# Optimization experiments

Measured on AMD Instinct MI355X. Metric: run time of the kernel, lower is better.

Reference implementation:

```python
import jax, jax.numpy as jnp
import numpy as np

B, T, F = 2, 128, 88          # batch, time frames, pitch bins (hard-coded 88)
HIDDEN = 64                    # LSTM input dim
N_UNIT = 64                    # channel dim (= 2 * lstm hidden 32)
N_HEAD = 4
HEAD_DIM = N_UNIT // N_HEAD    # 16
WINDOW = 7
N_LAYERS = 2
DIFF_STEPS = 100
LSTM_H = N_UNIT // 2           # 32 per direction


def setup_inputs() -> dict:
    key = jax.random.key(0)
    ks = jax.random.split(key, 12)
    s = 0.05
    inp = {
        'x': jax.random.normal(ks[0], (B, T * F, HIDDEN), jnp.float32),
        't': jax.random.randint(ks[1], (B,), 0, DIFF_STEPS, jnp.int32),
        # LSTM params, stacked [layer, direction, ...]; layer-1 input dim == 2*LSTM_H == HIDDEN
        'lstm_w_ih': s * jax.random.normal(ks[2], (N_LAYERS, 2, 4 * LSTM_H, HIDDEN), jnp.float32),
        'lstm_w_hh': s * jax.random.normal(ks[3], (N_LAYERS, 2, 4 * LSTM_H, LSTM_H), jnp.float32),
        'lstm_b_ih': s * jax.random.normal(ks[4], (N_LAYERS, 2, 4 * LSTM_H), jnp.float32),
        'lstm_b_hh': s * jax.random.normal(ks[5], (N_LAYERS, 2, 4 * LSTM_H), jnp.float32),
        # per-NA-layer params
        't_emb': s * jax.random.normal(ks[6], (N_LAYERS, DIFF_STEPS, N_UNIT), jnp.float32),
        'w_qkv': s * jax.random.normal(ks[7], (N_LAYERS, N_UNIT, 3 * N_UNIT), jnp.float32),
        'b_qkv': jnp.zeros((N_LAYERS, 3 * N_UNIT), jnp.float32),
        'rpb': s * jax.random.normal(ks[8], (N_LAYERS, N_HEAD, 2 * WINDOW - 1, 2 * WINDOW - 1), jnp.float32),
        'w_proj': s * jax.random.normal(ks[9], (N_LAYERS, N_UNIT, N_UNIT), jnp.float32),
        'b_proj': jnp.zeros((N_LAYERS, N_UNIT), jnp.float32),
    }
    return inp


def _lstm_dir(x, w_ih, w_hh, b_ih, b_hh, reverse):
    # x: [N, T, D]; pytorch gate order i, f, g, o
    N = x.shape[0]
    H = w_hh.shape[1]
    xs = jnp.swapaxes(x, 0, 1)
    if reverse:
        xs = xs[::-1]
    b = b_ih + b_hh
    def step(carry, xt):
        h, c = carry
        g = xt @ w_ih.T + h @ w_hh.T + b
        i, f, gg, o = jnp.split(g, 4, axis=-1)
        c = jax.nn.sigmoid(f) * c + jax.nn.sigmoid(i) * jnp.tanh(gg)
        h = jax.nn.sigmoid(o) * jnp.tanh(c)
        return (h, c), h
    h0 = jnp.zeros((N, H), x.dtype)
    _, hs = jax.lax.scan(step, (h0, h0), xs)
    if reverse:
        hs = hs[::-1]
    return jnp.swapaxes(hs, 0, 1)


def _bilstm(x, w_ih, w_hh, b_ih, b_hh):
    for l in range(w_ih.shape[0]):
        fwd = _lstm_dir(x, w_ih[l, 0], w_hh[l, 0], b_ih[l, 0], b_hh[l, 0], False)
        bwd = _lstm_dir(x, w_ih[l, 1], w_hh[l, 1], b_ih[l, 1], b_hh[l, 1], True)
        x = jnp.concatenate([fwd, bwd], axis=-1)
    return x


def _nbh(L, w):
    # NATTEN-style clamped (non-shrinking) neighborhood window per axis
    i = jnp.arange(L)
    start = jnp.clip(i - w // 2, 0, L - w)
    idx = start[:, None] + jnp.arange(w)[None, :]   # [L, w] absolute neighbor idx
    rel = idx - i[:, None] + (w - 1)                # [L, w] rel-pos-bias idx in [0, 2w-2]
    return idx, rel


def _na2d(x, t_idx, emb, wqkv, bqkv, rpb_l, wproj, bproj):
    # x: [B, Th, Tw, C]; diffusion-step conditioning via learned embedding add
    Bx, Th, Tw, C = x.shape
    h = x + emb[t_idx][:, None, None, :]
    qkv = (h @ wqkv + bqkv).reshape(Bx, Th, Tw, 3, N_HEAD, HEAD_DIM)
    q = jnp.moveaxis(qkv[..., 0, :, :], 3, 1) * (HEAD_DIM ** -0.5)  # [B,h,Th,Tw,d]
    k = jnp.moveaxis(qkv[..., 1, :, :], 3, 1)
    v = jnp.moveaxis(qkv[..., 2, :, :], 3, 1)
    ih, rh = _nbh(Th, WINDOW)
    iw, rw = _nbh(Tw, WINDOW)
    # gather windowed neighbors: [B,h,Th,Tw,w,w,d]
    kn = k[:, :, ih[:, None, :, None], iw[None, :, None, :], :]
    vn = v[:, :, ih[:, None, :, None], iw[None, :, None, :], :]
    bias = rpb_l[:, rh[:, None, :, None], rw[None, :, None, :]]     # [h,Th,Tw,w,w]
    logits = jnp.einsum('bhijd,bhijkld->bhijkl', q, kn) + bias[None]
    attn = jax.nn.softmax(logits.reshape(Bx, N_HEAD, Th, Tw, -1), axis=-1).reshape(logits.shape)
    out = jnp.einsum('bhijkl,bhijkld->bhijd', attn, vn)             # [B,h,Th,Tw,d]
    out = jnp.moveaxis(out, 1, 3).reshape(Bx, Th, Tw, C)
    return out @ wproj + bproj


def reference(x, t, lstm_w_ih, lstm_w_hh, lstm_b_ih, lstm_b_hh,
              t_emb, w_qkv, b_qkv, rpb, w_proj, b_proj):
    Bx = x.shape[0]
    Hin = x.shape[-1]
    Tt = x.shape[1] // F
    h = x.reshape(Bx, Tt, F, Hin).transpose(0, 2, 1, 3).reshape(Bx * F, Tt, Hin)
    h = _bilstm(h, lstm_w_ih, lstm_w_hh, lstm_b_ih, lstm_b_hh)      # [B*88, T, n_unit]
    # -> [B, T, 88, n_unit] 2D grid (height=T, width=88)
    h = h.reshape(Bx, F, Tt, N_UNIT).transpose(0, 2, 1, 3)
    for l in range(N_LAYERS):
        h = h + _na2d(h, t, t_emb[l], w_qkv[l], b_qkv[l], rpb[l], w_proj[l], b_proj[l])
    return h
```

## Files before the change

### kernel.cpp

```cpp
#include <hip/hip_runtime.h>
#include <math.h>

#define B_ 2
#define T_ 128
#define F_ 88
#define HID 64
#define NU 64
#define NH 4
#define HD 16
#define LH 32
#define NSEQ (B_*F_)
#define NTOK (B_*T_*F_)
#define NPOS (T_*F_)

__device__ __forceinline__ float fsig(float x) {
    return __builtin_amdgcn_rcpf(1.0f + __expf(-x));
}
__device__ __forceinline__ float ftanh(float x) {
    return 2.0f * __builtin_amdgcn_rcpf(1.0f + __expf(-2.0f*x)) - 1.0f;
}
__device__ __forceinline__ float rdlane(float v, int l) {
    return __uint_as_float(__builtin_amdgcn_readlane(__float_as_uint(v), l));
}

template<int LAYER>
__global__ void __launch_bounds__(256, 2) gg_kernel(
    const float* __restrict__ xin,
    const float* __restrict__ w_ih,
    const float* __restrict__ b_ih,
    const float* __restrict__ b_hh,
    float* __restrict__ G)
{
    __shared__ __align__(16) float xts[32][68];
    __shared__ __align__(16) float wsh[256][68];
    __shared__ float bsh[256];
    const int s  = blockIdx.x;
    const int t0 = blockIdx.y * 32;
    const int b = s / F_, f = s % F_;
    const int tid = threadIdx.x;

    for (int n = tid; n < 32*64; n += 256) {
        const int tt = n >> 6, k = n & 63;
        xts[tt][k] = (LAYER == 0)
            ? xin[(((size_t)b*T_ + t0+tt)*F_ + f)*HID + k]
            : xin[((size_t)s*T_ + t0+tt)*HID + k];
    }
    for (int n = tid; n < 256*64; n += 256) {
        const int row = n >> 6, k = n & 63;
        wsh[row][k] = w_ih[((size_t)LAYER*256 + row)*HID + k];
    }
    bsh[tid] = b_ih[LAYER*256 + tid] + b_hh[LAYER*256 + tid];
    __syncthreads();

    const int lane = tid & 63;
    const int g    = tid >> 6;
    const int dir  = g >> 1;
    const int th   = g & 1;
    const int rowA = dir*128 + lane;
    const int rowB = dir*128 + 64 + lane;

    float accA[16] = {}, accB[16] = {};
    #pragma unroll 4
    for (int k4 = 0; k4 < 16; k4++) {
        const float4 wA = *(const float4*)&wsh[rowA][k4*4];
        const float4 wB = *(const float4*)&wsh[rowB][k4*4];
        #pragma unroll
        for (int tt = 0; tt < 16; tt++) {
            const float4 xv = *(const float4*)&xts[th*16+tt][k4*4];
            accA[tt] += wA.x*xv.x + wA.y*xv.y + wA.z*xv.z + wA.w*xv.w;
            accB[tt] += wB.x*xv.x + wB.y*xv.y + wB.z*xv.z + wB.w*xv.w;
        }
    }
    const float bA = bsh[rowA], bB = bsh[rowB];
    float2* gout = (float2*)G + ((size_t)(s*2+dir)*T_ + t0 + th*16)*64 + lane;
    #pragma unroll
    for (int tt = 0; tt < 16; tt++) {
        float2 o; o.x = accA[tt] + bA; o.y = accB[tt] + bB;
        gout[(size_t)tt*64] = o;
    }
}

template<int LAYER>
__global__ void __launch_bounds__(128, 1) lstm_rec(
    const float* __restrict__ G,
    const float* __restrict__ w_hh,
    float* __restrict__ outp)
{
    __shared__ float hbuf[T_][NU];
    const int s = blockIdx.x;
    const int b = s / F_, f = s % F_;
    const int lane = threadIdx.x & 63;
    const int dir  = threadIdx.x >> 6;

    float2 wh2[LH];
    {
        const float4* pa = (const float4*)(w_hh + ((size_t)(LAYER*2+dir)*128 + lane)*LH);
        const float4* pb = (const float4*)(w_hh + ((size_t)(LAYER*2+dir)*128 + 64 + lane)*LH);
        #pragma unroll
        for (int k4 = 0; k4 < LH/4; k4++) {
            float4 a = pa[k4], c4 = pb[k4];
            wh2[k4*4+0].x=a.x; wh2[k4*4+0].y=c4.x;
            wh2[k4*4+1].x=a.y; wh2[k4*4+1].y=c4.y;
            wh2[k4*4+2].x=a.z; wh2[k4*4+2].y=c4.z;
            wh2[k4*4+3].x=a.w; wh2[k4*4+3].y=c4.w;
        }
    }
    const float2* gp = (const float2*)G + (size_t)(s*2+dir)*T_*64 + lane;
    #define GTIME(st) (dir ? (T_-1-(st)) : (st))

    const float a1 = (lane < LH) ? 2.f : 1.f;
    const float c1 = (lane < LH) ? -1.f : 0.f;

    float h = 0.f, c = 0.f;

    #define STEP(gAv, gBv, stepi)                                            \
    {                                                                        \
        float aA0 = (gAv), aB0 = (gBv), aA1 = 0.f, aB1 = 0.f;                \
        _Pragma("unroll")                                                    \
        for (int k = 0; k < 16; k++) {                                       \
            const float hk  = rdlane(h, k);                                  \
            const float hk2 = rdlane(h, k+16);                               \
            aA0 += wh2[k].x*hk;      aB0 += wh2[k].y*hk;                     \
            aA1 += wh2[k+16].x*hk2;  aB1 += wh2[k+16].y*hk2;                 \
        }                                                                    \
        const float accA = aA0 + aA1, accB = aB0 + aB1;                      \
        const float e0 = fsig(accA);                      \
        const float e1 = fmaf(a1, fsig(a1*accB), c1);     \
        const float x0 = __shfl_xor(e0, 32, 64);        \
        const float x1 = __shfl_xor(e1, 32, 64);        \
        c = x0*c + e0*e1;                                                    \
        h = x1 * ftanh(c);                                                   \
        if (lane < LH) hbuf[GTIME(stepi)][dir*LH + lane] = h;                \
    }

    float2 A[4], Bf[4];
    #pragma unroll
    for (int i = 0; i < 4; i++) A[i]  = gp[(size_t)GTIME(i)*64];
    #pragma unroll
    for (int i = 0; i < 4; i++) Bf[i] = gp[(size_t)GTIME(4+i)*64];

    #pragma unroll 1
    for (int grp = 0; grp < 32; grp++) {
        float2 P[4];
        const int pf = (grp < 30 ? grp + 2 : 31) * 4;
        #pragma unroll
        for (int i = 0; i < 4; i++) P[i] = gp[(size_t)GTIME(pf+i)*64];
        #pragma unroll
        for (int i = 0; i < 4; i++) { STEP(A[i].x, A[i].y, grp*4 + i); }
        #pragma unroll
        for (int i = 0; i < 4; i++) { A[i] = Bf[i]; Bf[i] = P[i]; }
    }
    #undef STEP
    #undef GTIME
    __syncthreads();

    const int tid = threadIdx.x;
    const float4* lds4 = (const float4*)&hbuf[0][0];
    if (LAYER == 0) {
        float4* out4 = (float4*)outp + (size_t)s*T_*16;
        #pragma unroll
        for (int it = 0; it < 16; it++)
            out4[it*128 + tid] = lds4[it*128 + tid];
    } else {
        const int c4 = tid & 15, trow = tid >> 4;
        #pragma unroll
        for (int it = 0; it < 16; it++) {
            const int t = it*8 + trow;
            ((float4*)outp)[(((size_t)b*T_ + t)*F_ + f)*16 + c4] = lds4[t*16 + c4];
        }
    }
}

__global__ void __launch_bounds__(256, 2) qkv_kernel(
    const float* __restrict__ hcur,
    const int*   __restrict__ tarr,
    const float* __restrict__ t_emb,
    const float* __restrict__ w_qkv,
    const float* __restrict__ b_qkv,
    const int layer,
    float* __restrict__ qb, float* __restrict__ kb, float* __restrict__ vb)
{
    __shared__ float as[64][65];
    __shared__ float wsh[64][64];
    const int m0 = blockIdx.x * 64;
    const int which = blockIdx.y;
    const int tid = threadIdx.x;
    const int bidx = m0 / NPOS;
    const int tb = tarr[bidx];
    const float* embp = t_emb + ((size_t)layer*100 + tb)*HID;

    for (int n = tid; n < 64*64; n += 256) {
        const int mm = n >> 6, k = n & 63;
        as[mm][k]  = hcur[((size_t)m0+mm)*64 + k] + embp[k];
        wsh[mm][k] = w_qkv[((size_t)layer*64 + mm)*192 + which*64 + k];
    }
    __syncthreads();

    const int tm = tid >> 4, tn = tid & 15;
    float acc[4][4] = {};
    for (int k = 0; k < 64; k++) {
        const float a0 = as[tm*4+0][k];
        const float a1 = as[tm*4+1][k];
        const float a2 = as[tm*4+2][k];
        const float a3 = as[tm*4+3][k];
        const float4 w = *(const float4*)&wsh[k][tn*4];
        acc[0][0]+=a0*w.x; acc[0][1]+=a0*w.y; acc[0][2]+=a0*w.z; acc[0][3]+=a0*w.w;
        acc[1][0]+=a1*w.x; acc[1][1]+=a1*w.y; acc[1][2]+=a1*w.z; acc[1][3]+=a1*w.w;
        acc[2][0]+=a2*w.x; acc[2][1]+=a2*w.y; acc[2][2]+=a2*w.z; acc[2][3]+=a2*w.w;
        acc[3][0]+=a3*w.x; acc[3][1]+=a3*w.y; acc[3][2]+=a3*w.z; acc[3][3]+=a3*w.w;
    }

    float* dst = (which == 0) ? qb : (which == 1) ? kb : vb;
    const float scale = (which == 0) ? 0.25f : 1.0f;
    const int hh = tn >> 2;
    const int dbase = (tn & 3) * 4;
    const float4 bv = *(const float4*)&b_qkv[(size_t)layer*192 + which*64 + tn*4];
    #pragma unroll
    for (int r = 0; r < 4; r++) {
        const int row = m0 + tm*4 + r;
        const int pos = row - bidx*NPOS;
        float4 o;
        o.x = (acc[r][0] + bv.x) * scale;
        o.y = (acc[r][1] + bv.y) * scale;
        o.z = (acc[r][2] + bv.z) * scale;
        o.w = (acc[r][3] + bv.w) * scale;
        *(float4*)&dst[(((size_t)bidx*NH + hh)*NPOS + pos)*HD + dbase] = o;
    }
}

__global__ void __launch_bounds__(192, 1) nattn_kernel(
    const float* __restrict__ qb,
    const float* __restrict__ kb,
    const float* __restrict__ vb,
    const float* __restrict__ rpb,
    const int layer,
    float* __restrict__ ao)
{
    __shared__ float ks[8][88][20];
    __shared__ float rp[169];
    const int blk = blockIdx.x;
    const int bh = blk & 7;
    const int it = blk >> 3;
    const int i0 = it*2;
    const int h  = bh & 3;
    const int bb = bh >> 2;
    const int tid = threadIdx.x;
    const int rs = min(max(i0-3, 0), T_-8);
    const float* kbase = kb + (size_t)bh*NPOS*HD;
    const float* vbase = vb + (size_t)bh*NPOS*HD;

    const bool act = (tid < 2*F_);
    const int isub = act ? (tid / F_) : 0;
    const int j    = act ? (tid - isub*F_) : 0;
    const int i    = i0 + isub;
    const int ihs  = min(max(i-3, 0), T_-7);
    const int ro   = ihs - rs;
    const int cw   = min(max(j-3, 0), F_-7);

    float4 q0, q1, q2, q3;
    if (act) {
        const float4* qp = (const float4*)&qb[((size_t)bh*NPOS + i*F_ + j)*HD];
        q0 = qp[0]; q1 = qp[1]; q2 = qp[2]; q3 = qp[3];
    }
    for (int n = tid; n < 169; n += 192)
        rp[n] = rpb[((size_t)layer*NH + h)*169 + n];
    for (int n4 = tid; n4 < 8*88*4; n4 += 192) {
        const int d4   = n4 & 3;
        const int rest = n4 >> 2;
        const int c    = rest % 88;
        const int r    = rest / 88;
        *(float4*)&ks[r][c][d4*4] =
            *(const float4*)&kbase[((size_t)(rs+r)*F_ + c)*HD + d4*4];
    }
    __syncthreads();

    float lg[49];
    if (act) {
        #pragma unroll
        for (int ki = 0; ki < 7; ki++) {
            const int rh = ihs + ki - i + 6;
            #pragma unroll
            for (int kj = 0; kj < 7; kj++) {
                const float4* kp = (const float4*)&ks[ro+ki][cw+kj][0];
                const float4 k0 = kp[0], k1 = kp[1], k2 = kp[2], k3 = kp[3];
                float d = q0.x*k0.x + q0.y*k0.y + q0.z*k0.z + q0.w*k0.w
                        + q1.x*k1.x + q1.y*k1.y + q1.z*k1.z + q1.w*k1.w
                        + q2.x*k2.x + q2.y*k2.y + q2.z*k2.z + q2.w*k2.w
                        + q3.x*k3.x + q3.y*k3.y + q3.z*k3.z + q3.w*k3.w;
                lg[ki*7+kj] = d + rp[rh*13 + (cw + kj - j + 6)];
            }
        }
        float m = lg[0];
        #pragma unroll
        for (int n = 1; n < 49; n++) m = fmaxf(m, lg[n]);
        float ssum = 0.f;
        #pragma unroll
        for (int n = 0; n < 49; n++) { lg[n] = __expf(lg[n] - m); ssum += lg[n]; }
        const float inv = __builtin_amdgcn_rcpf(ssum);
        #pragma unroll
        for (int n = 0; n < 49; n++) lg[n] *= inv;
    }
    __syncthreads();
    for (int n4 = tid; n4 < 8*88*4; n4 += 192) {
        const int d4   = n4 & 3;
        const int rest = n4 >> 2;
        const int c    = rest % 88;
        const int r    = rest / 88;
        *(float4*)&ks[r][c][d4*4] =
            *(const float4*)&vbase[((size_t)(rs+r)*F_ + c)*HD + d4*4];
    }
    __syncthreads();
    if (act) {
        float4 o0 = {0,0,0,0}, o1 = {0,0,0,0}, o2 = {0,0,0,0}, o3 = {0,0,0,0};
        #pragma unroll
        for (int ki = 0; ki < 7; ki++) {
            #pragma unroll
            for (int kj = 0; kj < 7; kj++) {
                const float a = lg[ki*7+kj];
                const float4* vp = (const float4*)&ks[ro+ki][cw+kj][0];
                const float4 v0 = vp[0], v1 = vp[1], v2 = vp[2], v3 = vp[3];
                o0.x += a*v0.x; o0.y += a*v0.y; o0.z += a*v0.z; o0.w += a*v0.w;
                o1.x += a*v1.x; o1.y += a*v1.y; o1.z += a*v1.z; o1.w += a*v1.w;
                o2.x += a*v2.x; o2.y += a*v2.y; o2.z += a*v2.z; o2.w += a*v2.w;
                o3.x += a*v3.x; o3.y += a*v3.y; o3.z += a*v3.z; o3.w += a*v3.w;
            }
        }
        float4* op = (float4*)&ao[(((size_t)bb*T_ + i)*F_ + j)*NU + h*HD];
        op[0]=o0; op[1]=o1; op[2]=o2; op[3]=o3;
    }
}

__global__ void __launch_bounds__(256, 2) proj_kernel(
    const float* __restrict__ ain,
    const float* __restrict__ hres,
    const float* __restrict__ w_proj,
    const float* __restrict__ b_proj,
    const int layer,
    float* __restrict__ outp)
{
    __shared__ float as[64][65];
    __shared__ float wsh[64][64];
    const int m0 = blockIdx.x * 64;
    const int tid = threadIdx.x;
    for (int n = tid; n < 64*64; n += 256) {
        const int mm = n >> 6, k = n & 63;
        as[mm][k]  = ain[((size_t)m0+mm)*64 + k];
        wsh[mm][k] = w_proj[(size_t)layer*4096 + n];
    }
    __syncthreads();
    const int tm = tid >> 4, tn = tid & 15;
    float acc[4][4] = {};
    for (int k = 0; k < 64; k++) {
        const float a0 = as[tm*4+0][k];
        const float a1 = as[tm*4+1][k];
        const float a2 = as[tm*4+2][k];
        const float a3 = as[tm*4+3][k];
        const float4 w = *(const float4*)&wsh[k][tn*4];
        acc[0][0]+=a0*w.x; acc[0][1]+=a0*w.y; acc[0][2]+=a0*w.z; acc[0][3]+=a0*w.w;
        acc[1][0]+=a1*w.x; acc[1][1]+=a1*w.y; acc[1][2]+=a1*w.z; acc[1][3]+=a1*w.w;
        acc[2][0]+=a2*w.x; acc[2][1]+=a2*w.y; acc[2][2]+=a2*w.z; acc[2][3]+=a2*w.w;
        acc[3][0]+=a3*w.x; acc[3][1]+=a3*w.y; acc[3][2]+=a3*w.z; acc[3][3]+=a3*w.w;
    }
    const float4 bv = *(const float4*)&b_proj[(size_t)layer*64 + tn*4];
    #pragma unroll
    for (int r = 0; r < 4; r++) {
        const int row = m0 + tm*4 + r;
        const float4 hv = *(const float4*)&hres[(size_t)row*64 + tn*4];
        float4 o;
        o.x = hv.x + acc[r][0] + bv.x;
        o.y = hv.y + acc[r][1] + bv.y;
        o.z = hv.z + acc[r][2] + bv.z;
        o.w = hv.w + acc[r][3] + bv.w;
        *(float4*)&outp[(size_t)row*64 + tn*4] = o;
    }
}

extern "C" void kernel_launch(void* const* d_in, const int* in_sizes, int n_in,
                              void* d_out, int out_size, void* d_ws, size_t ws_size,
                              hipStream_t stream) {
    const float* x      = (const float*)d_in[0];
    const int*   tarr   = (const int*)  d_in[1];
    const float* w_ih   = (const float*)d_in[2];
    const float* w_hh   = (const float*)d_in[3];
    const float* b_ih   = (const float*)d_in[4];
    const float* b_hh   = (const float*)d_in[5];
    const float* t_emb  = (const float*)d_in[6];
    const float* w_qkv  = (const float*)d_in[7];
    const float* b_qkv  = (const float*)d_in[8];
    const float* rpb    = (const float*)d_in[9];
    const float* w_proj = (const float*)d_in[10];
    const float* b_proj = (const float*)d_in[11];

    float* ws   = (float*)d_ws;
    const size_t CH = (size_t)NTOK * NU;
    float* hcur = ws;
    float* h0   = ws + CH;
    float* G    = ws + 2*CH;
    float* qbuf = ws + 2*CH;
    float* kbuf = ws + 3*CH;
    float* vbuf = ws + 4*CH;
    float* ao   = ws + 5*CH;
    float* outp = (float*)d_out;

    gg_kernel<0><<<dim3(NSEQ, T_/32), 256, 0, stream>>>(x,  w_ih, b_ih, b_hh, G);
    lstm_rec<0><<<NSEQ, 128, 0, stream>>>(G, w_hh, h0);
    gg_kernel<1><<<dim3(NSEQ, T_/32), 256, 0, stream>>>(h0, w_ih, b_ih, b_hh, G);
    lstm_rec<1><<<NSEQ, 128, 0, stream>>>(G, w_hh, hcur);

    for (int l = 0; l < 2; l++) {
        qkv_kernel<<<dim3(NTOK/64, 3), 256, 0, stream>>>(
            hcur, tarr, t_emb, w_qkv, b_qkv, l, qbuf, kbuf, vbuf);
        nattn_kernel<<<(T_/2)*8, 192, 0, stream>>>(
            qbuf, kbuf, vbuf, rpb, l, ao);
        proj_kernel<<<NTOK/64, 256, 0, stream>>>(
            ao, hcur, w_proj, b_proj, l, (l == 0) ? hcur : outp);
    }
}
```

Measured before the change: 260.1 us.

## Read K/V neighborhoods directly from global memory, one query row per block

Drops the shared-memory staging of an 8-row K/V tile in the neighborhood attention kernel. Each block now handles one query row (88 threads in a 128-thread block) and reads the 7x7 K and V neighbors straight from global memory, relying on L1/L2 caching for reuse. This removes the staging syncs and the large LDS footprint and doubles the block count. The cost is redundant global loads of overlapping neighborhoods and 40 idle lanes per block.

```diff
diff --git a/kernel.cpp b/kernel.cpp
--- a/kernel.cpp
+++ b/kernel.cpp
@@ -228,7 +228,7 @@
     }
 }
 
-__global__ void __launch_bounds__(192, 1) nattn_kernel(
+__global__ void __launch_bounds__(128, 2) nattn_kernel(
     const float* __restrict__ qb,
     const float* __restrict__ kb,
     const float* __restrict__ vb,
@@ -236,98 +236,70 @@
     const int layer,
     float* __restrict__ ao)
 {
-    __shared__ float ks[8][88][20];
     __shared__ float rp[169];
     const int blk = blockIdx.x;
     const int bh = blk & 7;
-    const int it = blk >> 3;
-    const int i0 = it*2;
+    const int i  = blk >> 3;
     const int h  = bh & 3;
     const int bb = bh >> 2;
     const int tid = threadIdx.x;
-    const int rs = min(max(i0-3, 0), T_-8);
+    const int ihs = min(max(i-3, 0), T_-7);
     const float* kbase = kb + (size_t)bh*NPOS*HD;
     const float* vbase = vb + (size_t)bh*NPOS*HD;
 
-    const bool act = (tid < 2*F_);
-    const int isub = act ? (tid / F_) : 0;
-    const int j    = act ? (tid - isub*F_) : 0;
-    const int i    = i0 + isub;
-    const int ihs  = min(max(i-3, 0), T_-7);
-    const int ro   = ihs - rs;
-    const int cw   = min(max(j-3, 0), F_-7);
-
-    float4 q0, q1, q2, q3;
-    if (act) {
-        const float4* qp = (const float4*)&qb[((size_t)bh*NPOS + i*F_ + j)*HD];
-        q0 = qp[0]; q1 = qp[1]; q2 = qp[2]; q3 = qp[3];
-    }
-    for (int n = tid; n < 169; n += 192)
+    for (int n = tid; n < 169; n += 128)
         rp[n] = rpb[((size_t)layer*NH + h)*169 + n];
-    for (int n4 = tid; n4 < 8*88*4; n4 += 192) {
-        const int d4   = n4 & 3;
-        const int rest = n4 >> 2;
-        const int c    = rest % 88;
-        const int r    = rest / 88;
-        *(float4*)&ks[r][c][d4*4] =
-            *(const float4*)&kbase[((size_t)(rs+r)*F_ + c)*HD + d4*4];
-    }
-    __syncthreads();
+    __syncthreads();
+
+    const int j = tid;
+    if (j >= F_) return;
+    const int cw = min(max(j-3, 0), F_-7);
+    const float4* qp = (const float4*)&qb[((size_t)bh*NPOS + i*F_ + j)*HD];
+    const float4 q0 = qp[0], q1 = qp[1], q2 = qp[2], q3 = qp[3];
 
     float lg[49];
-    if (act) {
-        #pragma unroll
-        for (int ki = 0; ki < 7; ki++) {
-            const int rh = ihs + ki - i + 6;
-            #pragma unroll
-            for (int kj = 0; kj < 7; kj++) {
-                const float4* kp = (const float4*)&ks[ro+ki][cw+kj][0];
-                const float4 k0 = kp[0], k1 = kp[1], k2 = kp[2], k3 = kp[3];
-                float d = q0.x*k0.x + q0.y*k0.y + q0.z*k0.z + q0.w*k0.w
-                        + q1.x*k1.x + q1.y*k1.y + q1.z*k1.z + q1.w*k1.w
-                        + q2.x*k2.x + q2.y*k2.y + q2.z*k2.z + q2.w*k2.w
-                        + q3.x*k3.x + q3.y*k3.y + q3.z*k3.z + q3.w*k3.w;
-                lg[ki*7+kj] = d + rp[rh*13 + (cw + kj - j + 6)];
-            }
-        }
-        float m = lg[0];
-        #pragma unroll
-        for (int n = 1; n < 49; n++) m = fmaxf(m, lg[n]);
-        float ssum = 0.f;
-        #pragma unroll
-        for (int n = 0; n < 49; n++) { lg[n] = __expf(lg[n] - m); ssum += lg[n]; }
-        const float inv = __builtin_amdgcn_rcpf(ssum);
-        #pragma unroll
-        for (int n = 0; n < 49; n++) lg[n] *= inv;
-    }
-    __syncthreads();
-    for (int n4 = tid; n4 < 8*88*4; n4 += 192) {
-        const int d4   = n4 & 3;
-        const int rest = n4 >> 2;
-        const int c    = rest % 88;
-        const int r    = rest / 88;
-        *(float4*)&ks[r][c][d4*4] =
-            *(const float4*)&vbase[((size_t)(rs+r)*F_ + c)*HD + d4*4];
-    }
-    __syncthreads();
-    if (act) {
-        float4 o0 = {0,0,0,0}, o1 = {0,0,0,0}, o2 = {0,0,0,0}, o3 = {0,0,0,0};
-        #pragma unroll
-        for (int ki = 0; ki < 7; ki++) {
-            #pragma unroll
-            for (int kj = 0; kj < 7; kj++) {
-                const float a = lg[ki*7+kj];
-                const float4* vp = (const float4*)&ks[ro+ki][cw+kj][0];
-                const float4 v0 = vp[0], v1 = vp[1], v2 = vp[2], v3 = vp[3];
-                o0.x += a*v0.x; o0.y += a*v0.y; o0.z += a*v0.z; o0.w += a*v0.w;
-                o1.x += a*v1.x; o1.y += a*v1.y; o1.z += a*v1.z; o1.w += a*v1.w;
-                o2.x += a*v2.x; o2.y += a*v2.y; o2.z += a*v2.z; o2.w += a*v2.w;
-                o3.x += a*v3.x; o3.y += a*v3.y; o3.z += a*v3.z; o3.w += a*v3.w;
-            }
-        }
-        float4* op = (float4*)&ao[(((size_t)bb*T_ + i)*F_ + j)*NU + h*HD];
-        op[0]=o0; op[1]=o1; op[2]=o2; op[3]=o3;
-    }
+    #pragma unroll
+    for (int ki = 0; ki < 7; ki++) {
+        const int rh = ihs + ki - i + 6;
+        const float* krow = &kbase[((size_t)(ihs+ki)*F_ + cw)*HD];
+        #pragma unroll
+        for (int kj = 0; kj < 7; kj++) {
+            const float4* kp = (const float4*)&krow[kj*HD];
+            const float4 k0 = kp[0], k1 = kp[1], k2 = kp[2], k3 = kp[3];
+            float d = q0.x*k0.x + q0.y*k0.y + q0.z*k0.z + q0.w*k0.w
+                    + q1.x*k1.x + q1.y*k1.y + q1.z*k1.z + q1.w*k1.w
+                    + q2.x*k2.x + q2.y*k2.y + q2.z*k2.z + q2.w*k2.w
+                    + q3.x*k3.x + q3.y*k3.y + q3.z*k3.z + q3.w*k3.w;
+            lg[ki*7+kj] = d + rp[rh*13 + (cw + kj - j + 6)];
+        }
+    }
+    float m = lg[0];
+    #pragma unroll
+    for (int n = 1; n < 49; n++) m = fmaxf(m, lg[n]);
+    float ssum = 0.f;
+    #pragma unroll
+    for (int n = 0; n < 49; n++) { lg[n] = __expf(lg[n] - m); ssum += lg[n]; }
+    const float inv = __builtin_amdgcn_rcpf(ssum);
+    #pragma unroll
+    for (int n = 0; n < 49; n++) lg[n] *= inv;
+
+    float4 o0 = {0,0,0,0}, o1 = {0,0,0,0}, o2 = {0,0,0,0}, o3 = {0,0,0,0};
+    #pragma unroll
+    for (int ki = 0; ki < 7; ki++) {
+        const float* vrow = &vbase[((size_t)(ihs+ki)*F_ + cw)*HD];
+        #pragma unroll
+        for (int kj = 0; kj < 7; kj++) {
+            const float a = lg[ki*7+kj];
+            const float4* vp = (const float4*)&vrow[kj*HD];
+            const float4 v0 = vp[0], v1 = vp[1], v2 = vp[2], v3 = vp[3];
+            o0.x += a*v0.x; o0.y += a*v0.y; o0.z += a*v0.z; o0.w += a*v0.w;
+            o1.x += a*v1.x; o1.y += a*v1.y; o1.z += a*v1.z; o1.w += a*v1.w;
+            o2.x += a*v2.x; o2.y += a*v2.y; o2.z += a*v2.z; o2.w += a*v2.w;
+            o3.x += a*v3.x; o3.y += a*v3.y; o3.z += a*v3.z; o3.w += a*v3.w;
+        }
+    }
+    float4* op = (float4*)&ao[(((size_t)bb*T_ + i)*F_ + j)*NU + h*HD];
+    op[0]=o0; op[1]=o1; op[2]=o2; op[3]=o3;
 }
 
 __global__ void __launch_bounds__(256, 2) proj_kernel(
@@ -410,7 +382,7 @@
     for (int l = 0; l < 2; l++) {
         qkv_kernel<<<dim3(NTOK/64, 3), 256, 0, stream>>>(
             hcur, tarr, t_emb, w_qkv, b_qkv, l, qbuf, kbuf, vbuf);
-        nattn_kernel<<<(T_/2)*8, 192, 0, stream>>>(
+        nattn_kernel<<<T_*8, 128, 0, stream>>>(
             qbuf, kbuf, vbuf, rpb, l, ao);
         proj_kernel<<<NTOK/64, 256, 0, stream>>>(
             ao, hcur, w_proj, b_proj, l, (l == 0) ? hcur : outp);
```

Result: slower. 299.2 us (+15.0%).
